# Optimization experiments

Hardware: AMD Instinct MI355X
Metric: run time of the kernel (lower is better)

The kernel has to match this reference:

```python
import jax, jax.numpy as jnp
import numpy as np


def setup_inputs() -> dict:
    key = jax.random.key(0)
    k1, k2 = jax.random.split(key)
    B, S, K, N = 2, 4096, 4096, 4096
    x = jax.random.randint(k1, (B, S, K), -127, 128, dtype=jnp.int32).astype(jnp.int8)
    weight = jax.random.randint(k2, (N, K), -127, 128, dtype=jnp.int32).astype(jnp.int8)
    bias = jnp.zeros((1, N), dtype=jnp.int8)
    a = jnp.float32(0.01)   # alpha = input_scale * weight_scale / output_scale
    b = jnp.float32(1.0)    # beta = bias_scale / output_scale
    return {"x": x, "weight": weight, "bias": bias, "a": a, "b": b}


def reference(x, weight, bias, a, b):
    # i8gemm.linear_a8_w8_b8_o8: int8 GEMM with int32 accumulation, then
    # y_int8 = saturate_cast(round(alpha * acc + beta * bias)).
    x_shape = x.shape
    xf = x.reshape(-1, x_shape[-1])                     # [M, K] int8
    acc = jnp.matmul(xf, weight.T, preferred_element_type=jnp.int32)  # [M, N]
    y = a * acc.astype(jnp.float32) + b * bias.astype(jnp.float32)    # fused epilogue
    yq = jnp.clip(jnp.round(y), -128.0, 127.0).astype(jnp.int8)       # requantize o8
    return yq.reshape(*x_shape[:-1], -1)
```

## Files before the change

kernel.cpp:

```cpp
#include <hip/hip_runtime.h>
#include <stdint.h>

#define M_DIM 8192
#define N_DIM 4096
#define K_DIM 4096

using int4v = __attribute__((ext_vector_type(4))) int;

__global__ __launch_bounds__(256) void pack_kernel(const int4* __restrict__ sx,
                                                   const int4* __restrict__ sw,
                                                   unsigned int* __restrict__ dst,
                                                   int nx, int ntot) {
    int idx = blockIdx.x * blockDim.x + threadIdx.x;
    if (idx >= ntot) return;
    int4 v = (idx < nx) ? sx[idx] : sw[idx - nx];
    dst[idx] = (v.x & 0xff) | ((v.y & 0xff) << 8) | ((v.z & 0xff) << 16) |
               ((v.w & 0xff) << 24);
}

__device__ __forceinline__ void async_copy16(const char* g, char* l) {
    __builtin_amdgcn_global_load_lds(
        (const __attribute__((address_space(1))) char*)g,
        (__attribute__((address_space(3))) char*)l, 16, 0, 0);
}

__global__ __launch_bounds__(512, 2) void gemm_i8_kernel(
    const char* __restrict__ Aq,
    const char* __restrict__ Bq,
    const int* __restrict__ bias,
    const float* __restrict__ a_ptr,
    const float* __restrict__ b_ptr,
    int32_t* __restrict__ out)
{
    __shared__ char As0[256 * 128];
    __shared__ char As1[256 * 128];
    __shared__ char Bs0[256 * 128];
    __shared__ char Bs1[256 * 128];

    const int tid  = threadIdx.x;
    const int lane = tid & 63;
    const int wave = tid >> 6;
    const int wr   = wave >> 2;
    const int wc   = wave & 3;

    const int bid = blockIdx.x;
    const int xcd = bid & 7;
    const int lin = bid >> 3;
    const int tile_m = (xcd & 3) * 8 + (lin & 7);
    const int tile_n = (xcd >> 2) * 8 + (lin >> 3);
    const int m0 = tile_m * 256;
    const int n0 = tile_n * 256;

    const float alpha = *a_ptr;
    const float beta  = *b_ptr;

    int4v acc[8][4] = {};

    const int fr = lane & 15;
    const int gw = lane >> 4;
    const int swz = (fr >> 1) & 7;
    const int k0off = (gw ^ swz) << 4;
    const int k1off = ((4 + gw) ^ swz) << 4;
    const int arow = wr * 128 + fr;
    const int brow = wc * 64 + fr;

    const int srow = tid >> 3;
    const int scg  = ((tid & 7) ^ ((tid >> 4) & 7)) << 4;
    const char* gA0 = Aq + (size_t)(m0 + srow) * K_DIM + scg;
    const char* gA1 = gA0 + (size_t)64 * K_DIM;
    const char* gB0 = Bq + (size_t)(n0 + srow) * K_DIM + scg;
    const char* gB1 = gB0 + (size_t)64 * K_DIM;

#define STAGE_TILE(AS, BS, t)                                                \
    {                                                                        \
        const size_t offL = (size_t)(t) * 128;                               \
        const size_t offH = (size_t)128 * K_DIM + (size_t)(t) * 128;         \
        async_copy16(gA0 + offL, &AS[(tid << 4)]);                           \
        async_copy16(gA1 + offL, &AS[(tid << 4) + 8192]);                    \
        async_copy16(gA0 + offH, &AS[16384 + (tid << 4)]);                   \
        async_copy16(gA1 + offH, &AS[16384 + (tid << 4) + 8192]);            \
        async_copy16(gB0 + offL, &BS[(tid << 4)]);                           \
        async_copy16(gB1 + offL, &BS[(tid << 4) + 8192]);                    \
        async_copy16(gB0 + offH, &BS[16384 + (tid << 4)]);                   \
        async_copy16(gB1 + offH, &BS[16384 + (tid << 4) + 8192]);            \
    }

#define COMPUTE_TILE(AS, BS)                                                 \
    {                                                                        \
        int4v a0[8], b0[4], a1[8], b1[4];                                    \
        _Pragma("unroll") for (int i = 0; i < 8; ++i)                        \
            a0[i] = *(const int4v*)&AS[(arow + i * 16) * 128 + k0off];       \
        _Pragma("unroll") for (int j = 0; j < 4; ++j)                        \
            b0[j] = *(const int4v*)&BS[(brow + j * 16) * 128 + k0off];       \
        _Pragma("unroll") for (int i = 0; i < 8; ++i)                        \
            a1[i] = *(const int4v*)&AS[(arow + i * 16) * 128 + k1off];       \
        _Pragma("unroll") for (int j = 0; j < 4; ++j)                        \
            b1[j] = *(const int4v*)&BS[(brow + j * 16) * 128 + k1off];       \
        __builtin_amdgcn_s_setprio(1);                                       \
        _Pragma("unroll") for (int i = 0; i < 8; ++i)                        \
        _Pragma("unroll") for (int j = 0; j < 4; ++j)                        \
            acc[i][j] = __builtin_amdgcn_mfma_i32_16x16x64_i8(               \
                a0[i], b0[j], acc[i][j], 0, 0, 0);                           \
        _Pragma("unroll") for (int i = 0; i < 8; ++i)                        \
        _Pragma("unroll") for (int j = 0; j < 4; ++j)                        \
            acc[i][j] = __builtin_amdgcn_mfma_i32_16x16x64_i8(               \
                a1[i], b1[j], acc[i][j], 0, 0, 0);                           \
        __builtin_amdgcn_s_setprio(0);                                       \
    }

#define SGB(mask, n) __builtin_amdgcn_sched_group_barrier(mask, n, 0)
#define SGB_PATTERN                                                          \
    {                                                                        \
        SGB(0x100, 12);                                                      \
        _Pragma("unroll") for (int r_ = 0; r_ < 12; ++r_) {                  \
            SGB(0x100, 1);                                                   \
            SGB(0x8, 2);                                                     \
        }                                                                    \
        SGB(0x8, 40);                                                        \
    }

#define TILE_END                                                             \
    {                                                                        \
        asm volatile("s_waitcnt vmcnt(0)" ::: "memory");                     \
        __builtin_amdgcn_s_barrier();                                        \
        __builtin_amdgcn_sched_barrier(0);                                   \
    }

    STAGE_TILE(As0, Bs0, 0);
    TILE_END;

#pragma unroll 1
    for (int it = 0; it < 15; ++it) {
        STAGE_TILE(As1, Bs1, 2 * it + 1);
        __builtin_amdgcn_sched_barrier(0);
        COMPUTE_TILE(As0, Bs0);
        SGB_PATTERN;
        TILE_END;
        STAGE_TILE(As0, Bs0, 2 * it + 2);
        __builtin_amdgcn_sched_barrier(0);
        COMPUTE_TILE(As1, Bs1);
        SGB_PATTERN;
        TILE_END;
    }
    STAGE_TILE(As1, Bs1, 31);
    __builtin_amdgcn_sched_barrier(0);
    COMPUTE_TILE(As0, Bs0);
    SGB_PATTERN;
    TILE_END;
    COMPUTE_TILE(As1, Bs1);

    const int orow = (lane >> 4) * 4;
    const int ocol = lane & 15;
#pragma unroll
    for (int j = 0; j < 4; ++j) {
        const int gn = n0 + wc * 64 + j * 16 + ocol;
        const float bb = beta * (float)bias[gn];
#pragma unroll
        for (int i = 0; i < 8; ++i) {
            const int gm = m0 + wr * 128 + i * 16 + orow;
#pragma unroll
            for (int r = 0; r < 4; ++r) {
                float v = alpha * (float)acc[i][j][r] + bb;
                v = rintf(v);
                v = fminf(fmaxf(v, -128.0f), 127.0f);
                out[(size_t)(gm + r) * N_DIM + gn] = (int32_t)v;
            }
        }
    }
}

extern "C" void kernel_launch(void* const* d_in, const int* in_sizes, int n_in,
                              void* d_out, int out_size, void* d_ws, size_t ws_size,
                              hipStream_t stream) {
    const int*   x    = (const int*)d_in[0];
    const int*   w    = (const int*)d_in[1];
    const int*   bias = (const int*)d_in[2];
    const float* a    = (const float*)d_in[3];
    const float* b    = (const float*)d_in[4];
    int32_t*     out  = (int32_t*)d_out;

    char* xq = (char*)d_ws;
    const int nx   = (M_DIM * K_DIM) / 4;
    const int nw   = (N_DIM * K_DIM) / 4;
    const int ntot = nx + nw;
    pack_kernel<<<(ntot + 255) / 256, 256, 0, stream>>>(
        (const int4*)x, (const int4*)w, (unsigned int*)xq, nx, ntot);

    char* wq = xq + (size_t)M_DIM * K_DIM;

    dim3 grid((M_DIM / 256) * (N_DIM / 256));
    gemm_i8_kernel<<<grid, 512, 0, stream>>>(xq, wq, bias, a, b, out);
}
```

Before: 398.8 us.

## Load B fragments directly from global into registers, drop B LDS staging

B operand fragments are now loaded by each wave directly from global memory into registers, one tile ahead, instead of being staged through double-buffered shared memory. Only A stays in LDS. This halves LDS usage and LDS read traffic, and the vmcnt waits are restructured to overlap the B register prefetch with the MFMAs. In exchange each B row is read by both row-waves without LDS reuse (more global/L2 traffic), the 16-byte per-lane global loads are less coalesced, and the previous MFMA/DS interleave scheduling hints are removed.

New measurement: 447.2 us. 12.2% more time.

```diff
diff --git a/kernel.cpp b/kernel.cpp
--- a/kernel.cpp
+++ b/kernel.cpp
@@ -34,8 +34,6 @@
 {
     __shared__ char As0[256 * 128];
     __shared__ char As1[256 * 128];
-    __shared__ char Bs0[256 * 128];
-    __shared__ char Bs1[256 * 128];
 
     const int tid  = threadIdx.x;
     const int lane = tid & 63;
@@ -55,6 +53,7 @@
     const float beta  = *b_ptr;
 
     int4v acc[8][4] = {};
+    int4v br[8];
 
     const int fr = lane & 15;
     const int gw = lane >> 4;
@@ -62,16 +61,15 @@
     const int k0off = (gw ^ swz) << 4;
     const int k1off = ((4 + gw) ^ swz) << 4;
     const int arow = wr * 128 + fr;
-    const int brow = wc * 64 + fr;
+
+    const char* gBf = Bq + (size_t)(n0 + wc * 64 + fr) * K_DIM + gw * 16;
 
     const int srow = tid >> 3;
     const int scg  = ((tid & 7) ^ ((tid >> 4) & 7)) << 4;
     const char* gA0 = Aq + (size_t)(m0 + srow) * K_DIM + scg;
     const char* gA1 = gA0 + (size_t)64 * K_DIM;
-    const char* gB0 = Bq + (size_t)(n0 + srow) * K_DIM + scg;
-    const char* gB1 = gB0 + (size_t)64 * K_DIM;
 
-#define STAGE_TILE(AS, BS, t)                                                \
+#define STAGE_A_TILE(AS, t)                                                  \
     {                                                                        \
         const size_t offL = (size_t)(t) * 128;                               \
         const size_t offH = (size_t)128 * K_DIM + (size_t)(t) * 128;         \
@@ -79,75 +77,64 @@
         async_copy16(gA1 + offL, &AS[(tid << 4) + 8192]);                    \
         async_copy16(gA0 + offH, &AS[16384 + (tid << 4)]);                   \
         async_copy16(gA1 + offH, &AS[16384 + (tid << 4) + 8192]);            \
-        async_copy16(gB0 + offL, &BS[(tid << 4)]);                           \
-        async_copy16(gB1 + offL, &BS[(tid << 4) + 8192]);                    \
-        async_copy16(gB0 + offH, &BS[16384 + (tid << 4)]);                   \
-        async_copy16(gB1 + offH, &BS[16384 + (tid << 4) + 8192]);            \
     }
 
-#define COMPUTE_TILE(AS, BS)                                                 \
+#define LOAD_B_KS(t, ks)                                                     \
     {                                                                        \
-        int4v a0[8], b0[4], a1[8], b1[4];                                    \
+        _Pragma("unroll") for (int j = 0; j < 4; ++j)                        \
+            br[j * 2 + (ks)] = *(const int4v*)(                              \
+                gBf + (size_t)(j * 16) * K_DIM + (size_t)(t) * 128 +         \
+                (ks) * 64);                                                  \
+        __builtin_amdgcn_sched_barrier(0);                                   \
+    }
+
+#define COMPUTE_KS(AS, ks, ko)                                               \
+    {                                                                        \
+        int4v a[8];                                                          \
         _Pragma("unroll") for (int i = 0; i < 8; ++i)                        \
-            a0[i] = *(const int4v*)&AS[(arow + i * 16) * 128 + k0off];       \
-        _Pragma("unroll") for (int j = 0; j < 4; ++j)                        \
-            b0[j] = *(const int4v*)&BS[(brow + j * 16) * 128 + k0off];       \
-        _Pragma("unroll") for (int i = 0; i < 8; ++i)                        \
-            a1[i] = *(const int4v*)&AS[(arow + i * 16) * 128 + k1off];       \
-        _Pragma("unroll") for (int j = 0; j < 4; ++j)                        \
-            b1[j] = *(const int4v*)&BS[(brow + j * 16) * 128 + k1off];       \
+            a[i] = *(const int4v*)&AS[(arow + i * 16) * 128 + (ko)];         \
         __builtin_amdgcn_s_setprio(1);                                       \
         _Pragma("unroll") for (int i = 0; i < 8; ++i)                        \
         _Pragma("unroll") for (int j = 0; j < 4; ++j)                        \
             acc[i][j] = __builtin_amdgcn_mfma_i32_16x16x64_i8(               \
-                a0[i], b0[j], acc[i][j], 0, 0, 0);                           \
-        _Pragma("unroll") for (int i = 0; i < 8; ++i)                        \
-        _Pragma("unroll") for (int j = 0; j < 4; ++j)                        \
-            acc[i][j] = __builtin_amdgcn_mfma_i32_16x16x64_i8(               \
-                a1[i], b1[j], acc[i][j], 0, 0, 0);                           \
+                a[i], br[j * 2 + (ks)], acc[i][j], 0, 0, 0);                 \
         __builtin_amdgcn_s_setprio(0);                                       \
     }
 
-#define SGB(mask, n) __builtin_amdgcn_sched_group_barrier(mask, n, 0)
-#define SGB_PATTERN                                                          \
+#define BODY(CUR, NXT, t)                                                    \
     {                                                                        \
-        SGB(0x100, 12);                                                      \
-        _Pragma("unroll") for (int r_ = 0; r_ < 12; ++r_) {                  \
-            SGB(0x100, 1);                                                   \
-            SGB(0x8, 2);                                                     \
-        }                                                                    \
-        SGB(0x8, 40);                                                        \
+        asm volatile("s_waitcnt vmcnt(4)" ::: "memory");                     \
+        __builtin_amdgcn_s_barrier();                                        \
+        __builtin_amdgcn_sched_barrier(0);                                   \
+        STAGE_A_TILE(NXT, (t) + 1);                                          \
+        __builtin_amdgcn_sched_barrier(0);                                   \
+        COMPUTE_KS(CUR, 0, k0off);                                           \
+        LOAD_B_KS((t) + 1, 0);                                               \
+        asm volatile("s_waitcnt vmcnt(8)" ::: "memory");                     \
+        __builtin_amdgcn_sched_barrier(0);                                   \
+        COMPUTE_KS(CUR, 1, k1off);                                           \
+        LOAD_B_KS((t) + 1, 1);                                               \
     }
 
-#define TILE_END                                                             \
-    {                                                                        \
-        asm volatile("s_waitcnt vmcnt(0)" ::: "memory");                     \
-        __builtin_amdgcn_s_barrier();                                        \
-        __builtin_amdgcn_sched_barrier(0);                                   \
-    }
-
-    STAGE_TILE(As0, Bs0, 0);
-    TILE_END;
+    STAGE_A_TILE(As0, 0);
+    LOAD_B_KS(0, 0);
+    LOAD_B_KS(0, 1);
 
 #pragma unroll 1
-    for (int it = 0; it < 15; ++it) {
-        STAGE_TILE(As1, Bs1, 2 * it + 1);
+    for (int i = 0; i < 15; ++i) {
+        BODY(As0, As1, 2 * i);
+        BODY(As1, As0, 2 * i + 1);
+    }
+    BODY(As0, As1, 30);
+    {
+        asm volatile("s_waitcnt vmcnt(4)" ::: "memory");
+        __builtin_amdgcn_s_barrier();
         __builtin_amdgcn_sched_barrier(0);
-        COMPUTE_TILE(As0, Bs0);
-        SGB_PATTERN;
-        TILE_END;
-        STAGE_TILE(As0, Bs0, 2 * it + 2);
+        COMPUTE_KS(As1, 0, k0off);
+        asm volatile("s_waitcnt vmcnt(0)" ::: "memory");
         __builtin_amdgcn_sched_barrier(0);
-        COMPUTE_TILE(As1, Bs1);
-        SGB_PATTERN;
-        TILE_END;
+        COMPUTE_KS(As1, 1, k1off);
     }
-    STAGE_TILE(As1, Bs1, 31);
-    __builtin_amdgcn_sched_barrier(0);
-    COMPUTE_TILE(As0, Bs0);
-    SGB_PATTERN;
-    TILE_END;
-    COMPUTE_TILE(As1, Bs1);
 
     const int orow = (lane >> 4) * 4;
     const int ocol = lane & 15;
```
